# Performance work log

Measured on AMD Instinct MI355X. Metric: run time of the kernel, lower is better.

## Reference

```python
import jax, jax.numpy as jnp
import numpy as np

N_PTS = 700000   # points
N_VOX = 250000   # occupied voxels
M_SP = 20000     # superpoints
GRID = 128       # spatial_shape per axis
C_IN = 6
C = 32           # media
BLOCK_REPS = 2
EPS = 1e-4       # BatchNorm eps


def _subm_conv(x, W, nbr):
    # x: [N_VOX, Cin], W: [27, Cin, Cout], nbr: [N_VOX, 27] (-1 = missing neighbor)
    mask = (nbr >= 0)
    g = x[jnp.clip(nbr, 0)] * mask[..., None].astype(x.dtype)  # [N_VOX, 27, Cin]
    return jnp.einsum('nkc,kcd->nd', g, W)


def _bn_eval(x, gamma, beta):
    # eval-mode BatchNorm1d with running_mean=0, running_var=1 (fresh init, module.eval())
    return x * (gamma / jnp.sqrt(1.0 + EPS)) + beta


def _segment_mean(x, seg, n):
    s = jax.ops.segment_sum(x, seg, num_segments=n)
    c = jax.ops.segment_sum(jnp.ones((x.shape[0], 1), x.dtype), seg, num_segments=n)
    return s / jnp.maximum(c, 1.0)


def setup_inputs() -> dict:
    rng = np.random.default_rng(0)
    # unique occupied voxel coordinates on a GRID^3 lattice
    ids = rng.choice(GRID ** 3, size=N_VOX, replace=False)
    coords = np.stack(np.unravel_index(ids, (GRID, GRID, GRID)), axis=1).astype(np.int64)
    lut = -np.ones(GRID ** 3, dtype=np.int64)
    lut[ids] = np.arange(N_VOX)
    off = np.stack(np.meshgrid(*([np.arange(-1, 2)] * 3), indexing='ij'), -1).reshape(-1, 3)  # [27,3]
    nc = coords[:, None, :] + off[None]                      # [N_VOX,27,3]
    valid = np.all((nc >= 0) & (nc < GRID), axis=-1)
    lin = (nc[..., 0] * GRID + nc[..., 1]) * GRID + nc[..., 2]
    nbr = np.where(valid, lut[np.clip(lin, 0, GRID ** 3 - 1)], -1).astype(np.int32)
    # every voxel gets >=1 point; every superpoint gets >=1 point
    p2v = rng.permutation(np.concatenate([np.arange(N_VOX), rng.integers(0, N_VOX, N_PTS - N_VOX)])).astype(np.int32)
    sp = rng.permutation(np.concatenate([np.arange(M_SP), rng.integers(0, M_SP, N_PTS - M_SP)])).astype(np.int32)
    key = jax.random.key(0)
    k1, k2, k3 = jax.random.split(key, 3)
    feats = jax.random.normal(k1, (N_PTS, C_IN), jnp.float32)
    W_in = jax.random.normal(k2, (27, C_IN, C), jnp.float32) * 0.1
    W_blocks = jax.random.normal(k3, (BLOCK_REPS, 2, 27, C, C), jnp.float32) * 0.05
    bn_gamma = jnp.ones((5, C), jnp.float32)
    bn_beta = jnp.zeros((5, C), jnp.float32)
    return {'feats': feats, 'W_in': W_in, 'W_blocks': W_blocks,
            'bn_gamma': bn_gamma, 'bn_beta': bn_beta,
            'p2v_map': jnp.asarray(p2v), 'neighbor_idx': jnp.asarray(nbr),
            'superpoints': jnp.asarray(sp)}


def reference(feats, W_in, W_blocks, bn_gamma, bn_beta, p2v_map, neighbor_idx, superpoints):
    # voxelization: mean of point feats per voxel (pointgroup_ops.voxelization)
    vox = _segment_mean(feats, p2v_map, N_VOX)            # [N_VOX, 6]
    # input_conv: SubMConv3d(6->32, k=3, bias=False)
    x = _subm_conv(vox, W_in, neighbor_idx)               # [N_VOX, 32]
    # UBlock(nPlanes=[32]) == block_reps pre-activation ResidualBlocks
    for r in range(BLOCK_REPS):
        h = x
        y = jax.nn.relu(_bn_eval(x, bn_gamma[2 * r], bn_beta[2 * r]))
        y = _subm_conv(y, W_blocks[r, 0], neighbor_idx)
        y = jax.nn.relu(_bn_eval(y, bn_gamma[2 * r + 1], bn_beta[2 * r + 1]))
        y = _subm_conv(y, W_blocks[r, 1], neighbor_idx)
        x = h + y  # identity shortcut (in_channels == out_channels)
    # output_layer: BN + ReLU
    x = jax.nn.relu(_bn_eval(x, bn_gamma[4], bn_beta[4]))
    # devoxelize: gather per-point voxel features, then scatter_mean over superpoints
    pt = x[p2v_map]                                        # [N_PTS, 32]
    return _segment_mean(pt, superpoints, M_SP)            # [M_SP, 32]
```

## Files before the change

kernel.cpp:

```cpp
#include <hip/hip_runtime.h>

#define N_PTS    700000
#define N_VOXELS 250000
#define M_SP     20000
#define EPS_BN   1e-4f
#define NB_V     245
#define NB_S     20
#define BKT_V    62
#define BKT_S    79

typedef __attribute__((ext_vector_type(8))) short  bf16x8;
typedef __attribute__((ext_vector_type(8))) ushort u16x8;
typedef __attribute__((ext_vector_type(4))) float  f32x4;

__device__ __forceinline__ ushort f2bf(float f) {
    unsigned u = __float_as_uint(f);
    return (ushort)((u + 0x7FFFu + ((u >> 16) & 1u)) >> 16);
}
__device__ __forceinline__ float bf2f(ushort h) {
    return __uint_as_float(((unsigned)h) << 16);
}

__global__ __launch_bounds__(256) void k_hist2(const int* __restrict__ p2v,
                                               const int* __restrict__ sp,
                                               int* __restrict__ cnt_v,
                                               int* __restrict__ cnt_s) {
    int i = blockIdx.x * 256 + threadIdx.x;
    if (i < N_PTS) {
        atomicAdd(&cnt_v[p2v[i]], 1);
        atomicAdd(&cnt_s[sp[i]], 1);
    }
}

__global__ __launch_bounds__(256) void k_part2(const int* __restrict__ cnt_v,
                                               const int* __restrict__ cnt_s,
                                               int* __restrict__ psum_v,
                                               int* __restrict__ psum_s) {
    __shared__ int l[256];
    int b = blockIdx.x, t = threadIdx.x;
    const int* cnt; int* psum; int n, bb;
    if (b < NB_V) { cnt = cnt_v; psum = psum_v; n = N_VOXELS; bb = b; }
    else          { cnt = cnt_s; psum = psum_s; n = M_SP;     bb = b - NB_V; }
    int base = bb * 1024 + t * 4;
    int s = 0;
    #pragma unroll
    for (int j = 0; j < 4; ++j) { int i = base + j; if (i < n) s += cnt[i]; }
    l[t] = s; __syncthreads();
    for (int st = 128; st > 0; st >>= 1) {
        if (t < st) l[t] += l[t + st];
        __syncthreads();
    }
    if (t == 0) psum[bb] = l[0];
}

__global__ __launch_bounds__(256) void k_scan2(int* __restrict__ psum_v,
                                               int* __restrict__ psum_s) {
    __shared__ int l[256];
    int t = threadIdx.x;
    int* psum = blockIdx.x == 0 ? psum_v : psum_s;
    int nb    = blockIdx.x == 0 ? NB_V : NB_S;
    int orig = (t < nb) ? psum[t] : 0;
    l[t] = orig; __syncthreads();
    for (int st = 1; st < 256; st <<= 1) {
        int v = (t >= st) ? l[t - st] : 0;
        __syncthreads();
        l[t] += v;
        __syncthreads();
    }
    if (t < nb) psum[t] = l[t] - orig;
}

__global__ __launch_bounds__(256) void k_excl2(const int* __restrict__ cnt_v,
                                               const int* __restrict__ cnt_s,
                                               const int* __restrict__ psum_v,
                                               const int* __restrict__ psum_s,
                                               int* __restrict__ off_v,
                                               int* __restrict__ off_s,
                                               int* __restrict__ cur_v,
                                               int* __restrict__ cur_s) {
    __shared__ int l[256];
    int b = blockIdx.x, t = threadIdx.x;
    const int* cnt; const int* psum; int* off; int* cur; int n, bb;
    if (b < NB_V) { cnt = cnt_v; psum = psum_v; off = off_v; cur = cur_v; n = N_VOXELS; bb = b; }
    else          { cnt = cnt_s; psum = psum_s; off = off_s; cur = cur_s; n = M_SP;     bb = b - NB_V; }
    int base = bb * 1024 + t * 4;
    int c[4]; int s = 0;
    #pragma unroll
    for (int j = 0; j < 4; ++j) {
        int i = base + j;
        c[j] = (i < n) ? cnt[i] : 0;
        s += c[j];
    }
    int orig = s;
    l[t] = s; __syncthreads();
    for (int st = 1; st < 256; st <<= 1) {
        int v = (t >= st) ? l[t - st] : 0;
        __syncthreads();
        l[t] += v;
        __syncthreads();
    }
    int run = l[t] - orig + psum[bb];
    #pragma unroll
    for (int j = 0; j < 4; ++j) {
        int i = base + j;
        if (i < n) { off[i] = run; cur[i] = run; run += c[j]; }
    }
}

__global__ __launch_bounds__(256) void k_bcur_init(const int* __restrict__ off_v,
                                                   const int* __restrict__ off_s,
                                                   int* __restrict__ bcur_v,
                                                   int* __restrict__ bcur_s) {
    int t = threadIdx.x;
    if (t < BKT_V) bcur_v[t] = off_v[t << 12];
    if (t < BKT_S) bcur_s[t] = off_s[t << 8];
}

__global__ __launch_bounds__(256) void k_bucket(const int* __restrict__ p2v,
                                                const int* __restrict__ sp,
                                                int* __restrict__ bcur_v,
                                                int* __restrict__ bcur_s,
                                                int2* __restrict__ bufv,
                                                int2* __restrict__ bufs) {
    __shared__ int hv[BKT_V], hs[BKT_S];
    __shared__ int bv[BKT_V], bs[BKT_S];
    const int t = threadIdx.x;
    const int base = blockIdx.x * 1024;
    for (int i = t; i < BKT_V; i += 256) hv[i] = 0;
    for (int i = t; i < BKT_S; i += 256) hs[i] = 0;
    __syncthreads();
    int pv[4], ks[4], rv[4], rs[4];
    #pragma unroll
    for (int j = 0; j < 4; ++j) {
        int i = base + j * 256 + t;
        if (i < N_PTS) {
            pv[j] = p2v[i];
            ks[j] = sp[i];
            rv[j] = atomicAdd(&hv[pv[j] >> 12], 1);
            rs[j] = atomicAdd(&hs[ks[j] >> 8], 1);
        }
    }
    __syncthreads();
    for (int b = t; b < BKT_V; b += 256) bv[b] = atomicAdd(&bcur_v[b], hv[b]);
    for (int b = t; b < BKT_S; b += 256) bs[b] = atomicAdd(&bcur_s[b], hs[b]);
    __syncthreads();
    #pragma unroll
    for (int j = 0; j < 4; ++j) {
        int i = base + j * 256 + t;
        if (i < N_PTS) {
            int2 ev; ev.x = i;     ev.y = pv[j];
            int2 es; es.x = pv[j]; es.y = ks[j];
            bufv[bv[pv[j] >> 12] + rv[j]] = ev;
            bufs[bs[ks[j] >> 8] + rs[j]] = es;
        }
    }
}

#define PL_SL 4
__global__ __launch_bounds__(256) void k_place(const int* __restrict__ off_v,
                                               const int* __restrict__ off_s,
                                               int* __restrict__ cur_v,
                                               int* __restrict__ cur_s,
                                               const int2* __restrict__ bufv,
                                               const int2* __restrict__ bufs,
                                               int* __restrict__ pidx_v,
                                               int* __restrict__ pidx_s) {
    int blk = blockIdx.x;
    const int2* buf; int* cur; int* pidx; int s, e;
    if (blk < BKT_V * PL_SL) {
        int b = blk / PL_SL;
        s = off_v[b << 12];
        e = ((b + 1) << 12 >= N_VOXELS) ? N_PTS : off_v[(b + 1) << 12];
        buf = bufv; cur = cur_v; pidx = pidx_v;
        int q = blk % PL_SL, len = e - s;
        int s0 = s + (len * q) / PL_SL, e0 = s + (len * (q + 1)) / PL_SL;
        s = s0; e = e0;
    } else {
        blk -= BKT_V * PL_SL;
        int b = blk / PL_SL;
        s = off_s[b << 8];
        e = ((b + 1) << 8 >= M_SP) ? N_PTS : off_s[(b + 1) << 8];
        buf = bufs; cur = cur_s; pidx = pidx_s;
        int q = blk % PL_SL, len = e - s;
        int s0 = s + (len * q) / PL_SL, e0 = s + (len * (q + 1)) / PL_SL;
        s = s0; e = e0;
    }
    for (int i = s + threadIdx.x; i < e; i += 256) {
        int2 en = buf[i];
        pidx[atomicAdd(&cur[en.y], 1)] = en.x;
    }
}

__global__ __launch_bounds__(256) void k_vox_gather(const float* __restrict__ feats,
                                                    const int* __restrict__ off,
                                                    const int* __restrict__ cnt,
                                                    const int* __restrict__ pidx,
                                                    ushort* __restrict__ voxH,
                                                    ushort* __restrict__ voxL) {
    int v = blockIdx.x * 256 + threadIdx.x;
    if (v >= N_VOXELS) return;
    int s = off[v], c = cnt[v];
    float a[6] = {0, 0, 0, 0, 0, 0};
    for (int k = 0; k < c; ++k) {
        int p = pidx[s + k];
        const float2* f = (const float2*)(feats + (size_t)p * 6);
        float2 x0 = f[0], x1 = f[1], x2 = f[2];
        a[0] += x0.x; a[1] += x0.y; a[2] += x1.x;
        a[3] += x1.y; a[4] += x2.x; a[5] += x2.y;
    }
    float inv = 1.0f / (float)max(c, 1);
    u16x8 hv, lv;
    #pragma unroll
    for (int j = 0; j < 6; ++j) {
        float m = a[j] * inv;
        ushort h = f2bf(m);
        hv[j] = h;
        lv[j] = f2bf(m - bf2f(h));
    }
    hv[6] = 0; hv[7] = 0; lv[6] = 0; lv[7] = 0;
    *(u16x8*)(voxH + (size_t)v * 8) = hv;
    *(u16x8*)(voxL + (size_t)v * 8) = lv;
}

__global__ __launch_bounds__(256) void k_wprep_in(const float* __restrict__ W,
                                                  ushort* __restrict__ WbH,
                                                  ushort* __restrict__ WbL) {
    int t = blockIdx.x * 256 + threadIdx.x;
    if (t >= 7 * 2 * 64) return;
    int l  = t & 63;
    int nf = (t >> 6) & 1;
    int s7 = t >> 7;
    int g  = l >> 4;
    int c  = nf * 16 + (l & 15);
    int o  = s7 * 4 + g;
    u16x8 hv, lv;
    #pragma unroll
    for (int j = 0; j < 8; ++j) {
        float w = (j < 6 && o < 27) ? W[(o * 6 + j) * 32 + c] : 0.0f;
        ushort h = f2bf(w);
        hv[j] = h;
        lv[j] = f2bf(w - bf2f(h));
    }
    *(u16x8*)(WbH + (size_t)t * 8) = hv;
    *(u16x8*)(WbL + (size_t)t * 8) = lv;
}

__global__ __launch_bounds__(256) void k_wprep(const float* __restrict__ W,
                                               ushort* __restrict__ Wb) {
    int t = blockIdx.x * 256 + threadIdx.x;
    if (t >= 4 * 27 * 2 * 64) return;
    int l  = t & 63;
    int nf = (t >> 6) & 1;
    int co = t >> 7;
    const float* Wo = W + (size_t)co * 1024;
    int kb = (l >> 4) * 8;
    int c  = nf * 16 + (l & 15);
    u16x8 v;
    #pragma unroll
    for (int j = 0; j < 8; ++j) v[j] = f2bf(Wo[(kb + j) * 32 + c]);
    *(u16x8*)(Wb + (size_t)t * 8) = v;
}

__global__ __launch_bounds__(256) void k_conv_in_m(const ushort* __restrict__ voxH,
                                                   const ushort* __restrict__ voxL,
                                                   const int* __restrict__ nbr,
                                                   const ushort* __restrict__ WbH,
                                                   const ushort* __restrict__ WbL,
                                                   const float* __restrict__ gamma,
                                                   const float* __restrict__ beta,
                                                   float* __restrict__ x_out,
                                                   ushort* __restrict__ act_out) {
    __shared__ int nl[128][27];
    const int tid = threadIdx.x;
    const int vbase = blockIdx.x * 128;
    for (int i = tid; i < 128 * 27; i += 256) {
        int gi = vbase * 27 + i;
        nl[0][i] = (gi < N_VOXELS * 27) ? nbr[gi] : -1;
    }
    __syncthreads();

    const int l   = tid & 63;
    const int wav = tid >> 6;
    const int r   = l & 15;
    const int g   = l >> 4;
    const int vr0 = wav * 32 + r;
    const int vr1 = vr0 + 16;

    f32x4 a00 = {0,0,0,0}, a01 = {0,0,0,0}, a10 = {0,0,0,0}, a11 = {0,0,0,0};

    for (int s7 = 0; s7 < 7; ++s7) {
        int o = s7 * 4 + g;
        int n0 = (o < 27) ? nl[vr0][o] : -1;
        int n1 = (o < 27) ? nl[vr1][o] : -1;
        bf16x8 A0h = {0,0,0,0,0,0,0,0}, A0l = {0,0,0,0,0,0,0,0};
        bf16x8 A1h = {0,0,0,0,0,0,0,0}, A1l = {0,0,0,0,0,0,0,0};
        if (n0 >= 0) {
            A0h = *(const bf16x8*)(voxH + (size_t)n0 * 8);
            A0l = *(const bf16x8*)(voxL + (size_t)n0 * 8);
        }
        if (n1 >= 0) {
            A1h = *(const bf16x8*)(voxH + (size_t)n1 * 8);
            A1l = *(const bf16x8*)(voxL + (size_t)n1 * 8);
        }
        const bf16x8 B0h = *(const bf16x8*)(WbH + (size_t)(s7 * 2 + 0) * 512 + l * 8);
        const bf16x8 B1h = *(const bf16x8*)(WbH + (size_t)(s7 * 2 + 1) * 512 + l * 8);
        const bf16x8 B0l = *(const bf16x8*)(WbL + (size_t)(s7 * 2 + 0) * 512 + l * 8);
        const bf16x8 B1l = *(const bf16x8*)(WbL + (size_t)(s7 * 2 + 1) * 512 + l * 8);
        a00 = __builtin_amdgcn_mfma_f32_16x16x32_bf16(A0h, B0h, a00, 0, 0, 0);
        a00 = __builtin_amdgcn_mfma_f32_16x16x32_bf16(A0l, B0h, a00, 0, 0, 0);
        a00 = __builtin_amdgcn_mfma_f32_16x16x32_bf16(A0h, B0l, a00, 0, 0, 0);
        a01 = __builtin_amdgcn_mfma_f32_16x16x32_bf16(A0h, B1h, a01, 0, 0, 0);
        a01 = __builtin_amdgcn_mfma_f32_16x16x32_bf16(A0l, B1h, a01, 0, 0, 0);
        a01 = __builtin_amdgcn_mfma_f32_16x16x32_bf16(A0h, B1l, a01, 0, 0, 0);
        a10 = __builtin_amdgcn_mfma_f32_16x16x32_bf16(A1h, B0h, a10, 0, 0, 0);
        a10 = __builtin_amdgcn_mfma_f32_16x16x32_bf16(A1l, B0h, a10, 0, 0, 0);
        a10 = __builtin_amdgcn_mfma_f32_16x16x32_bf16(A1h, B0l, a10, 0, 0, 0);
        a11 = __builtin_amdgcn_mfma_f32_16x16x32_bf16(A1h, B1h, a11, 0, 0, 0);
        a11 = __builtin_amdgcn_mfma_f32_16x16x32_bf16(A1l, B1h, a11, 0, 0, 0);
        a11 = __builtin_amdgcn_mfma_f32_16x16x32_bf16(A1h, B1l, a11, 0, 0, 0);
    }

    const float rs  = rsqrtf(1.f + EPS_BN);
    const float sc0 = gamma[r] * rs,      bb0 = beta[r];
    const float sc1 = gamma[r + 16] * rs, bb1 = beta[r + 16];

    #pragma unroll
    for (int fr = 0; fr < 2; ++fr) {
        #pragma unroll
        for (int j = 0; j < 4; ++j) {
            int vv = vbase + wav * 32 + fr * 16 + g * 4 + j;
            if (vv >= N_VOXELS) continue;
            float v0 = fr ? a10[j] : a00[j];
            float v1 = fr ? a11[j] : a01[j];
            float* xp = x_out + (size_t)vv * 32;
            xp[r]      = v0;
            xp[r + 16] = v1;
            act_out[(size_t)vv * 32 + r]      = f2bf(fmaxf(v0 * sc0 + bb0, 0.f));
            act_out[(size_t)vv * 32 + r + 16] = f2bf(fmaxf(v1 * sc1 + bb1, 0.f));
        }
    }
}

__global__ __launch_bounds__(256) void k_conv32m(const ushort* __restrict__ act_in,
                                                 const int* __restrict__ nbr,
                                                 const ushort* __restrict__ Wb,
                                                 const float* __restrict__ gamma,
                                                 const float* __restrict__ beta,
                                                 float* __restrict__ x_inout,
                                                 ushort* __restrict__ act_out,
                                                 const int save_x) {
    __shared__ int nl[128][27];
    const int tid = threadIdx.x;
    const int vbase = blockIdx.x * 128;
    for (int i = tid; i < 128 * 27; i += 256) {
        int gi = vbase * 27 + i;
        nl[0][i] = (gi < N_VOXELS * 27) ? nbr[gi] : -1;
    }
    __syncthreads();

    const int l   = tid & 63;
    const int wav = tid >> 6;
    const int r   = l & 15;
    const int g   = l >> 4;
    const int vr0 = wav * 32 + r;
    const int vr1 = vr0 + 16;

    f32x4 a00 = {0,0,0,0}, a01 = {0,0,0,0}, a10 = {0,0,0,0}, a11 = {0,0,0,0};

    for (int o = 0; o < 27; ++o) {
        int n0 = nl[vr0][o];
        int n1 = nl[vr1][o];
        bf16x8 A0 = {0,0,0,0,0,0,0,0}, A1 = {0,0,0,0,0,0,0,0};
        if (n0 >= 0) A0 = *(const bf16x8*)(act_in + (size_t)n0 * 32 + g * 8);
        if (n1 >= 0) A1 = *(const bf16x8*)(act_in + (size_t)n1 * 32 + g * 8);
        const bf16x8 B0 = *(const bf16x8*)(Wb + (size_t)(o * 2 + 0) * 512 + l * 8);
        const bf16x8 B1 = *(const bf16x8*)(Wb + (size_t)(o * 2 + 1) * 512 + l * 8);
        a00 = __builtin_amdgcn_mfma_f32_16x16x32_bf16(A0, B0, a00, 0, 0, 0);
        a01 = __builtin_amdgcn_mfma_f32_16x16x32_bf16(A0, B1, a01, 0, 0, 0);
        a10 = __builtin_amdgcn_mfma_f32_16x16x32_bf16(A1, B0, a10, 0, 0, 0);
        a11 = __builtin_amdgcn_mfma_f32_16x16x32_bf16(A1, B1, a11, 0, 0, 0);
    }

    const float rs  = rsqrtf(1.f + EPS_BN);
    const float sc0 = gamma[r] * rs,      bb0 = beta[r];
    const float sc1 = gamma[r + 16] * rs, bb1 = beta[r + 16];

    #pragma unroll
    for (int fr = 0; fr < 2; ++fr) {
        #pragma unroll
        for (int j = 0; j < 4; ++j) {
            int vv = vbase + wav * 32 + fr * 16 + g * 4 + j;
            if (vv >= N_VOXELS) continue;
            float v0 = fr ? a10[j] : a00[j];
            float v1 = fr ? a11[j] : a01[j];
            if (x_inout) {
                float* xp = x_inout + (size_t)vv * 32;
                v0 += xp[r];
                v1 += xp[r + 16];
                if (save_x) {
                    xp[r]      = v0;
                    xp[r + 16] = v1;
                }
            }
            act_out[(size_t)vv * 32 + r]      = f2bf(fmaxf(v0 * sc0 + bb0, 0.f));
            act_out[(size_t)vv * 32 + r + 16] = f2bf(fmaxf(v1 * sc1 + bb1, 0.f));
        }
    }
}

__global__ __launch_bounds__(256) void k_sp_gather(const ushort* __restrict__ act,
                                                   const int* __restrict__ off,
                                                   const int* __restrict__ cnt,
                                                   const int* __restrict__ pidx,
                                                   float* __restrict__ out) {
    int sp = blockIdx.x * 4 + (threadIdx.x >> 6);
    if (sp >= M_SP) return;
    int l   = threadIdx.x & 63;
    int grp = l >> 4;
    int ch2 = l & 15;
    int s = off[sp], c = cnt[sp];
    float a0 = 0.f, a1 = 0.f;
    for (int j = s + grp; j < s + c; j += 4) {
        int v = pidx[j];
        unsigned pk = *(const unsigned*)(act + (size_t)v * 32 + ch2 * 2);
        a0 += __uint_as_float(pk << 16);
        a1 += __uint_as_float(pk & 0xFFFF0000u);
    }
    a0 += __shfl_xor(a0, 16); a1 += __shfl_xor(a1, 16);
    a0 += __shfl_xor(a0, 32); a1 += __shfl_xor(a1, 32);
    if (grp == 0) {
        float inv = 1.0f / (float)max(c, 1);
        *(float2*)(out + (size_t)sp * 32 + ch2 * 2) = make_float2(a0 * inv, a1 * inv);
    }
}

extern "C" void kernel_launch(void* const* d_in, const int* in_sizes, int n_in,
                              void* d_out, int out_size, void* d_ws, size_t ws_size,
                              hipStream_t stream) {
    const float* feats    = (const float*)d_in[0];
    const float* W_in     = (const float*)d_in[1];
    const float* W_blocks = (const float*)d_in[2];
    const float* gamma    = (const float*)d_in[3];
    const float* beta     = (const float*)d_in[4];
    const int*   p2v      = (const int*)d_in[5];
    const int*   nbr      = (const int*)d_in[6];
    const int*   sp       = (const int*)d_in[7];
    float* out = (float*)d_out;
    float* wsf = (float*)d_ws;

    int*    cnt_v  = (int*)(wsf + 0);
    int*    off_v  = (int*)(wsf + 250000);
    int*    cnt_s  = (int*)(wsf + 500000);
    int*    off_s  = (int*)(wsf + 520000);
    int*    psum_v = (int*)(wsf + 540000);
    int*    psum_s = (int*)(wsf + 541000);
    int*    cur_v  = (int*)(wsf + 542000);
    int*    cur_s  = (int*)(wsf + 792000);
    int*    bcur_v = (int*)(wsf + 812000);
    int*    bcur_s = (int*)(wsf + 813000);
    int*    pidx_v = (int*)(wsf + 814000);
    int*    pidx_s = (int*)(wsf + 1514000);
    ushort* WbH_in = (ushort*)(wsf + 2214000);
    ushort* WbL_in = (ushort*)(wsf + 2218000);
    ushort* Wb     = (ushort*)(wsf + 2222000);
    float*  x      = wsf + 2300000;
    int2*   bufv   = (int2*)(wsf + 2300000);
    int2*   bufs   = (int2*)(wsf + 3700000);
    ushort* actA   = (ushort*)(wsf + 10300000);
    ushort* actB   = (ushort*)(wsf + 14300000);
    ushort* voxH   = (ushort*)(wsf + 14300000);
    ushort* voxL   = (ushort*)(wsf + 15300000);

    const int GP = (N_PTS + 255) / 256;

    hipMemsetAsync(cnt_v, 0, N_VOXELS * sizeof(int), stream);
    hipMemsetAsync(cnt_s, 0, M_SP * sizeof(int), stream);

    k_wprep<<<(4 * 27 * 2 * 64 + 255) / 256, 256, 0, stream>>>(W_blocks, Wb);
    k_wprep_in<<<(7 * 2 * 64 + 255) / 256, 256, 0, stream>>>(W_in, WbH_in, WbL_in);

    k_hist2<<<GP, 256, 0, stream>>>(p2v, sp, cnt_v, cnt_s);
    k_part2<<<NB_V + NB_S, 256, 0, stream>>>(cnt_v, cnt_s, psum_v, psum_s);
    k_scan2<<<2, 256, 0, stream>>>(psum_v, psum_s);
    k_excl2<<<NB_V + NB_S, 256, 0, stream>>>(cnt_v, cnt_s, psum_v, psum_s,
                                             off_v, off_s, cur_v, cur_s);
    k_bcur_init<<<1, 256, 0, stream>>>(off_v, off_s, bcur_v, bcur_s);
    k_bucket<<<(N_PTS + 1023) / 1024, 256, 0, stream>>>(p2v, sp, bcur_v, bcur_s,
                                                        bufv, bufs);
    k_place<<<(BKT_V + BKT_S) * PL_SL, 256, 0, stream>>>(off_v, off_s, cur_v, cur_s,
                                                         bufv, bufs, pidx_v, pidx_s);

    k_vox_gather<<<(N_VOXELS + 255) / 256, 256, 0, stream>>>(feats, off_v, cnt_v,
                                                             pidx_v, voxH, voxL);

    const int CONV_GRID = (N_VOXELS + 127) / 128;
    k_conv_in_m<<<CONV_GRID, 256, 0, stream>>>(voxH, voxL, nbr, WbH_in, WbL_in,
                                               gamma + 0, beta + 0, x, actA);

    const int WBSZ = 27 * 2 * 64 * 8;
    k_conv32m<<<CONV_GRID, 256, 0, stream>>>(actA, nbr, Wb + 0 * WBSZ,
                                             gamma + 32, beta + 32, nullptr, actB, 0);
    k_conv32m<<<CONV_GRID, 256, 0, stream>>>(actB, nbr, Wb + 1 * WBSZ,
                                             gamma + 64, beta + 64, x, actA, 1);
    k_conv32m<<<CONV_GRID, 256, 0, stream>>>(actA, nbr, Wb + 2 * WBSZ,
                                             gamma + 96, beta + 96, nullptr, actB, 0);
    k_conv32m<<<CONV_GRID, 256, 0, stream>>>(actB, nbr, Wb + 3 * WBSZ,
                                             gamma + 128, beta + 128, x, actA, 0);

    k_sp_gather<<<(M_SP + 3) / 4, 256, 0, stream>>>(actA, off_s, cnt_s,
                                                    pidx_s, out);
}
```

Before: 465.1 us.

## Replace global per-key histogram and scans with bucket-level counting sort

Rebuilds the counting sort behind the voxel and superpoint CSR. A coarse bucket histogram is built with shared-memory atomics, scanned in one small kernel, and then each bucket block computes its own per-key histogram, local scan, offsets and placement in shared memory. This removes the global per-key atomics, the multi-kernel scan chain, the large memsets and the global cursor atomics. In exchange there are fewer but larger blocks in the finalize step, so a few long buckets could limit parallelism.

Result: faster. 386.1 us (-17.0%).

```diff
diff --git a/kernel.cpp b/kernel.cpp
--- a/kernel.cpp
+++ b/kernel.cpp
@@ -4,10 +4,10 @@
 #define N_VOXELS 250000
 #define M_SP     20000
 #define EPS_BN   1e-4f
-#define NB_V     245
-#define NB_S     20
-#define BKT_V    62
-#define BKT_S    79
+#define VSH      11
+#define SSH      7
+#define BKT_V    123
+#define BKT_S    157
 
 typedef __attribute__((ext_vector_type(8))) short  bf16x8;
 typedef __attribute__((ext_vector_type(8))) ushort u16x8;
@@ -21,45 +21,41 @@
     return __uint_as_float(((unsigned)h) << 16);
 }
 
-__global__ __launch_bounds__(256) void k_hist2(const int* __restrict__ p2v,
-                                               const int* __restrict__ sp,
-                                               int* __restrict__ cnt_v,
-                                               int* __restrict__ cnt_s) {
-    int i = blockIdx.x * 256 + threadIdx.x;
-    if (i < N_PTS) {
-        atomicAdd(&cnt_v[p2v[i]], 1);
-        atomicAdd(&cnt_s[sp[i]], 1);
-    }
-}
-
-__global__ __launch_bounds__(256) void k_part2(const int* __restrict__ cnt_v,
-                                               const int* __restrict__ cnt_s,
-                                               int* __restrict__ psum_v,
-                                               int* __restrict__ psum_s) {
-    __shared__ int l[256];
-    int b = blockIdx.x, t = threadIdx.x;
-    const int* cnt; int* psum; int n, bb;
-    if (b < NB_V) { cnt = cnt_v; psum = psum_v; n = N_VOXELS; bb = b; }
-    else          { cnt = cnt_s; psum = psum_s; n = M_SP;     bb = b - NB_V; }
-    int base = bb * 1024 + t * 4;
-    int s = 0;
-    #pragma unroll
-    for (int j = 0; j < 4; ++j) { int i = base + j; if (i < n) s += cnt[i]; }
-    l[t] = s; __syncthreads();
-    for (int st = 128; st > 0; st >>= 1) {
-        if (t < st) l[t] += l[t + st];
-        __syncthreads();
-    }
-    if (t == 0) psum[bb] = l[0];
-}
-
-__global__ __launch_bounds__(256) void k_scan2(int* __restrict__ psum_v,
-                                               int* __restrict__ psum_s) {
+__global__ __launch_bounds__(256) void k_bktcnt(const int* __restrict__ p2v,
+                                                const int* __restrict__ sp,
+                                                int* __restrict__ bkcnt_v,
+                                                int* __restrict__ bkcnt_s) {
+    __shared__ int hv[BKT_V], hs[BKT_S];
+    const int t = threadIdx.x;
+    const int base = blockIdx.x * 1024;
+    for (int i = t; i < BKT_V; i += 256) hv[i] = 0;
+    for (int i = t; i < BKT_S; i += 256) hs[i] = 0;
+    __syncthreads();
+    #pragma unroll
+    for (int j = 0; j < 4; ++j) {
+        int i = base + j * 256 + t;
+        if (i < N_PTS) {
+            atomicAdd(&hv[p2v[i] >> VSH], 1);
+            atomicAdd(&hs[sp[i] >> SSH], 1);
+        }
+    }
+    __syncthreads();
+    for (int b = t; b < BKT_V; b += 256) if (hv[b]) atomicAdd(&bkcnt_v[b], hv[b]);
+    for (int b = t; b < BKT_S; b += 256) if (hs[b]) atomicAdd(&bkcnt_s[b], hs[b]);
+}
+
+__global__ __launch_bounds__(256) void k_bktscan(const int* __restrict__ bkcnt_v,
+                                                 const int* __restrict__ bkcnt_s,
+                                                 int* __restrict__ bkbase_v,
+                                                 int* __restrict__ bkbase_s,
+                                                 int* __restrict__ bcur_v,
+                                                 int* __restrict__ bcur_s) {
     __shared__ int l[256];
     int t = threadIdx.x;
-    int* psum = blockIdx.x == 0 ? psum_v : psum_s;
-    int nb    = blockIdx.x == 0 ? NB_V : NB_S;
-    int orig = (t < nb) ? psum[t] : 0;
+    const int* cntb; int* base; int* cur; int nb;
+    if (blockIdx.x == 0) { cntb = bkcnt_v; base = bkbase_v; cur = bcur_v; nb = BKT_V; }
+    else                 { cntb = bkcnt_s; base = bkbase_s; cur = bcur_s; nb = BKT_S; }
+    int orig = (t < nb) ? cntb[t] : 0;
     l[t] = orig; __syncthreads();
     for (int st = 1; st < 256; st <<= 1) {
         int v = (t >= st) ? l[t - st] : 0;
@@ -67,53 +63,8 @@
         l[t] += v;
         __syncthreads();
     }
-    if (t < nb) psum[t] = l[t] - orig;
-}
-
-__global__ __launch_bounds__(256) void k_excl2(const int* __restrict__ cnt_v,
-                                               const int* __restrict__ cnt_s,
-                                               const int* __restrict__ psum_v,
-                                               const int* __restrict__ psum_s,
-                                               int* __restrict__ off_v,
-                                               int* __restrict__ off_s,
-                                               int* __restrict__ cur_v,
-                                               int* __restrict__ cur_s) {
-    __shared__ int l[256];
-    int b = blockIdx.x, t = threadIdx.x;
-    const int* cnt; const int* psum; int* off; int* cur; int n, bb;
-    if (b < NB_V) { cnt = cnt_v; psum = psum_v; off = off_v; cur = cur_v; n = N_VOXELS; bb = b; }
-    else          { cnt = cnt_s; psum = psum_s; off = off_s; cur = cur_s; n = M_SP;     bb = b - NB_V; }
-    int base = bb * 1024 + t * 4;
-    int c[4]; int s = 0;
-    #pragma unroll
-    for (int j = 0; j < 4; ++j) {
-        int i = base + j;
-        c[j] = (i < n) ? cnt[i] : 0;
-        s += c[j];
-    }
-    int orig = s;
-    l[t] = s; __syncthreads();
-    for (int st = 1; st < 256; st <<= 1) {
-        int v = (t >= st) ? l[t - st] : 0;
-        __syncthreads();
-        l[t] += v;
-        __syncthreads();
-    }
-    int run = l[t] - orig + psum[bb];
-    #pragma unroll
-    for (int j = 0; j < 4; ++j) {
-        int i = base + j;
-        if (i < n) { off[i] = run; cur[i] = run; run += c[j]; }
-    }
-}
-
-__global__ __launch_bounds__(256) void k_bcur_init(const int* __restrict__ off_v,
-                                                   const int* __restrict__ off_s,
-                                                   int* __restrict__ bcur_v,
-                                                   int* __restrict__ bcur_s) {
-    int t = threadIdx.x;
-    if (t < BKT_V) bcur_v[t] = off_v[t << 12];
-    if (t < BKT_S) bcur_s[t] = off_s[t << 8];
+    if (t < nb) { int b = l[t] - orig; base[t] = b; cur[t] = b; }
+    if (t == 0) base[nb] = N_PTS;
 }
 
 __global__ __launch_bounds__(256) void k_bucket(const int* __restrict__ p2v,
@@ -136,13 +87,13 @@
         if (i < N_PTS) {
             pv[j] = p2v[i];
             ks[j] = sp[i];
-            rv[j] = atomicAdd(&hv[pv[j] >> 12], 1);
-            rs[j] = atomicAdd(&hs[ks[j] >> 8], 1);
-        }
-    }
-    __syncthreads();
-    for (int b = t; b < BKT_V; b += 256) bv[b] = atomicAdd(&bcur_v[b], hv[b]);
-    for (int b = t; b < BKT_S; b += 256) bs[b] = atomicAdd(&bcur_s[b], hs[b]);
+            rv[j] = atomicAdd(&hv[pv[j] >> VSH], 1);
+            rs[j] = atomicAdd(&hs[ks[j] >> SSH], 1);
+        }
+    }
+    __syncthreads();
+    for (int b = t; b < BKT_V; b += 256) bv[b] = hv[b] ? atomicAdd(&bcur_v[b], hv[b]) : 0;
+    for (int b = t; b < BKT_S; b += 256) bs[b] = hs[b] ? atomicAdd(&bcur_s[b], hs[b]) : 0;
     __syncthreads();
     #pragma unroll
     for (int j = 0; j < 4; ++j) {
@@ -150,44 +101,72 @@
         if (i < N_PTS) {
             int2 ev; ev.x = i;     ev.y = pv[j];
             int2 es; es.x = pv[j]; es.y = ks[j];
-            bufv[bv[pv[j] >> 12] + rv[j]] = ev;
-            bufs[bs[ks[j] >> 8] + rs[j]] = es;
-        }
-    }
-}
-
-#define PL_SL 4
-__global__ __launch_bounds__(256) void k_place(const int* __restrict__ off_v,
-                                               const int* __restrict__ off_s,
-                                               int* __restrict__ cur_v,
-                                               int* __restrict__ cur_s,
-                                               const int2* __restrict__ bufv,
-                                               const int2* __restrict__ bufs,
-                                               int* __restrict__ pidx_v,
-                                               int* __restrict__ pidx_s) {
-    int blk = blockIdx.x;
-    const int2* buf; int* cur; int* pidx; int s, e;
-    if (blk < BKT_V * PL_SL) {
-        int b = blk / PL_SL;
-        s = off_v[b << 12];
-        e = ((b + 1) << 12 >= N_VOXELS) ? N_PTS : off_v[(b + 1) << 12];
-        buf = bufv; cur = cur_v; pidx = pidx_v;
-        int q = blk % PL_SL, len = e - s;
-        int s0 = s + (len * q) / PL_SL, e0 = s + (len * (q + 1)) / PL_SL;
-        s = s0; e = e0;
+            bufv[bv[pv[j] >> VSH] + rv[j]] = ev;
+            bufs[bs[ks[j] >> SSH] + rs[j]] = es;
+        }
+    }
+}
+
+__global__ __launch_bounds__(256) void k_fin(const int* __restrict__ bkbase_v,
+                                             const int* __restrict__ bkbase_s,
+                                             const int2* __restrict__ bufv,
+                                             const int2* __restrict__ bufs,
+                                             int* __restrict__ pidx_v,
+                                             int* __restrict__ pidx_s,
+                                             int* __restrict__ cnt_v,
+                                             int* __restrict__ cnt_s,
+                                             int* __restrict__ off_v,
+                                             int* __restrict__ off_s) {
+    __shared__ int hist[1 << VSH];
+    __shared__ int lsum[256];
+    const int blk = blockIdx.x, t = threadIdx.x;
+    const int2* buf; int* pidx; int* cnt; int* off;
+    int kbase, nk, s, e;
+    if (blk < BKT_V) {
+        buf = bufv; pidx = pidx_v; cnt = cnt_v; off = off_v;
+        kbase = blk << VSH; nk = min(1 << VSH, N_VOXELS - kbase);
+        s = bkbase_v[blk]; e = bkbase_v[blk + 1];
     } else {
-        blk -= BKT_V * PL_SL;
-        int b = blk / PL_SL;
-        s = off_s[b << 8];
-        e = ((b + 1) << 8 >= M_SP) ? N_PTS : off_s[(b + 1) << 8];
-        buf = bufs; cur = cur_s; pidx = pidx_s;
-        int q = blk % PL_SL, len = e - s;
-        int s0 = s + (len * q) / PL_SL, e0 = s + (len * (q + 1)) / PL_SL;
-        s = s0; e = e0;
-    }
-    for (int i = s + threadIdx.x; i < e; i += 256) {
+        int b = blk - BKT_V;
+        buf = bufs; pidx = pidx_s; cnt = cnt_s; off = off_s;
+        kbase = b << SSH; nk = min(1 << SSH, M_SP - kbase);
+        s = bkbase_s[b]; e = bkbase_s[b + 1];
+    }
+    for (int i = t; i < nk; i += 256) hist[i] = 0;
+    __syncthreads();
+    for (int i = s + t; i < e; i += 256) atomicAdd(&hist[buf[i].y - kbase], 1);
+    __syncthreads();
+    int c[8], ls = 0;
+    #pragma unroll
+    for (int j = 0; j < 8; ++j) {
+        int idx = t * 8 + j;
+        c[j] = (idx < nk) ? hist[idx] : 0;
+        ls += c[j];
+    }
+    lsum[t] = ls;
+    __syncthreads();
+    for (int st = 1; st < 256; st <<= 1) {
+        int v = (t >= st) ? lsum[t - st] : 0;
+        __syncthreads();
+        lsum[t] += v;
+        __syncthreads();
+    }
+    int run = lsum[t] - ls;
+    #pragma unroll
+    for (int j = 0; j < 8; ++j) {
+        int idx = t * 8 + j;
+        if (idx < nk) {
+            off[kbase + idx] = s + run;
+            cnt[kbase + idx] = c[j];
+            hist[idx] = run;
+            run += c[j];
+        }
+    }
+    __syncthreads();
+    for (int i = s + t; i < e; i += 256) {
         int2 en = buf[i];
-        pidx[atomicAdd(&cur[en.y], 1)] = en.x;
+        int pos = atomicAdd(&hist[en.y - kbase], 1);
+        pidx[s + pos] = en.x;
     }
 }
 
@@ -448,47 +427,43 @@
     float* out = (float*)d_out;
     float* wsf = (float*)d_ws;
 
-    int*    cnt_v  = (int*)(wsf + 0);
-    int*    off_v  = (int*)(wsf + 250000);
-    int*    cnt_s  = (int*)(wsf + 500000);
-    int*    off_s  = (int*)(wsf + 520000);
-    int*    psum_v = (int*)(wsf + 540000);
-    int*    psum_s = (int*)(wsf + 541000);
-    int*    cur_v  = (int*)(wsf + 542000);
-    int*    cur_s  = (int*)(wsf + 792000);
-    int*    bcur_v = (int*)(wsf + 812000);
-    int*    bcur_s = (int*)(wsf + 813000);
-    int*    pidx_v = (int*)(wsf + 814000);
-    int*    pidx_s = (int*)(wsf + 1514000);
-    ushort* WbH_in = (ushort*)(wsf + 2214000);
-    ushort* WbL_in = (ushort*)(wsf + 2218000);
-    ushort* Wb     = (ushort*)(wsf + 2222000);
-    float*  x      = wsf + 2300000;
-    int2*   bufv   = (int2*)(wsf + 2300000);
-    int2*   bufs   = (int2*)(wsf + 3700000);
-    ushort* actA   = (ushort*)(wsf + 10300000);
-    ushort* actB   = (ushort*)(wsf + 14300000);
-    ushort* voxH   = (ushort*)(wsf + 14300000);
-    ushort* voxL   = (ushort*)(wsf + 15300000);
-
-    const int GP = (N_PTS + 255) / 256;
-
-    hipMemsetAsync(cnt_v, 0, N_VOXELS * sizeof(int), stream);
-    hipMemsetAsync(cnt_s, 0, M_SP * sizeof(int), stream);
+    int*    cnt_v    = (int*)(wsf + 0);
+    int*    off_v    = (int*)(wsf + 250000);
+    int*    cnt_s    = (int*)(wsf + 500000);
+    int*    off_s    = (int*)(wsf + 520000);
+    int*    bkcnt_v  = (int*)(wsf + 540000);
+    int*    bkcnt_s  = (int*)(wsf + 540123);
+    int*    bkbase_v = (int*)(wsf + 541000);
+    int*    bkbase_s = (int*)(wsf + 541200);
+    int*    bcur_v   = (int*)(wsf + 541400);
+    int*    bcur_s   = (int*)(wsf + 541600);
+    int*    pidx_v   = (int*)(wsf + 542000);
+    int*    pidx_s   = (int*)(wsf + 1242000);
+    ushort* WbH_in   = (ushort*)(wsf + 1942000);
+    ushort* WbL_in   = (ushort*)(wsf + 1946000);
+    ushort* Wb       = (ushort*)(wsf + 1950000);
+    float*  x        = wsf + 2010000;
+    int2*   bufv     = (int2*)(wsf + 2010000);
+    int2*   bufs     = (int2*)(wsf + 3500000);
+    ushort* actA     = (ushort*)(wsf + 10010000);
+    ushort* actB     = (ushort*)(wsf + 14010000);
+    ushort* voxH     = (ushort*)(wsf + 14010000);
+    ushort* voxL     = (ushort*)(wsf + 15010000);
+
+    const int GB = (N_PTS + 1023) / 1024;
+
+    hipMemsetAsync(bkcnt_v, 0, (BKT_V + BKT_S) * sizeof(int), stream);
 
     k_wprep<<<(4 * 27 * 2 * 64 + 255) / 256, 256, 0, stream>>>(W_blocks, Wb);
     k_wprep_in<<<(7 * 2 * 64 + 255) / 256, 256, 0, stream>>>(W_in, WbH_in, WbL_in);
 
-    k_hist2<<<GP, 256, 0, stream>>>(p2v, sp, cnt_v, cnt_s);
-    k_part2<<<NB_V + NB_S, 256, 0, stream>>>(cnt_v, cnt_s, psum_v, psum_s);
-    k_scan2<<<2, 256, 0, stream>>>(psum_v, psum_s);
-    k_excl2<<<NB_V + NB_S, 256, 0, stream>>>(cnt_v, cnt_s, psum_v, psum_s,
-                                             off_v, off_s, cur_v, cur_s);
-    k_bcur_init<<<1, 256, 0, stream>>>(off_v, off_s, bcur_v, bcur_s);
-    k_bucket<<<(N_PTS + 1023) / 1024, 256, 0, stream>>>(p2v, sp, bcur_v, bcur_s,
-                                                        bufv, bufs);
-    k_place<<<(BKT_V + BKT_S) * PL_SL, 256, 0, stream>>>(off_v, off_s, cur_v, cur_s,
-                                                         bufv, bufs, pidx_v, pidx_s);
+    k_bktcnt<<<GB, 256, 0, stream>>>(p2v, sp, bkcnt_v, bkcnt_s);
+    k_bktscan<<<2, 256, 0, stream>>>(bkcnt_v, bkcnt_s, bkbase_v, bkbase_s,
+                                     bcur_v, bcur_s);
+    k_bucket<<<GB, 256, 0, stream>>>(p2v, sp, bcur_v, bcur_s, bufv, bufs);
+    k_fin<<<BKT_V + BKT_S, 256, 0, stream>>>(bkbase_v, bkbase_s, bufv, bufs,
+                                             pidx_v, pidx_s, cnt_v, cnt_s,
+                                             off_v, off_s);
 
     k_vox_gather<<<(N_VOXELS + 255) / 256, 256, 0, stream>>>(feats, off_v, cnt_v,
                                                              pidx_v, voxH, voxL);
```
